# Optimization experiments

Hardware: AMD Instinct MI355X
Metric: run time of the kernel (lower is better)

Reference implementation:

```python
import jax, jax.numpy as jnp
import numpy as np

LN_EPS = 1e-5

def _layernorm(x, w, b):
    mu = jnp.mean(x, axis=-1, keepdims=True)
    var = jnp.mean(jnp.square(x - mu), axis=-1, keepdims=True)
    return (x - mu) * jax.lax.rsqrt(var + LN_EPS) * w + b

def setup_inputs() -> dict:
    key = jax.random.key(0)
    ks = jax.random.split(key, 8)
    B, T, D, E = 8, 4096, 1024, 4
    inner = 4 * D
    x = jax.random.normal(ks[0], (B, T, D), dtype=jnp.float32)
    router_prob = jax.random.uniform(ks[1], (B, T, E), dtype=jnp.float32)
    alpha = jnp.ones((), dtype=jnp.float32)
    norm_w = jnp.ones((D,), dtype=jnp.float32)
    norm_b = jnp.zeros((D,), dtype=jnp.float32)
    l1_w = jax.random.normal(ks[2], (inner, D), dtype=jnp.float32) * 0.02
    l1_b = jax.random.normal(ks[3], (inner,), dtype=jnp.float32) * 0.02
    l2_w = jax.random.normal(ks[4], (D, inner), dtype=jnp.float32) * 0.02
    l2_b = jax.random.normal(ks[5], (D,), dtype=jnp.float32) * 0.02
    return {"x": x, "router_prob": router_prob, "alpha": alpha,
            "norm_w": norm_w, "norm_b": norm_b,
            "l1_w": l1_w, "l1_b": l1_b, "l2_w": l2_w, "l2_b": l2_b}

def reference(x, router_prob, alpha, norm_w, norm_b, l1_w, l1_b, l2_w, l2_b):
    B, T, D = x.shape
    E = router_prob.shape[2]
    n = T // E  # tokens per expert (contiguous slices)
    outs = []
    for e in range(E):  # small fixed loop; each expert has a different width m
        xs = x[:, e * n:(e + 1) * n, :]              # [B,n,D]
        h = _layernorm(xs, norm_w, norm_b)
        m = D // (2 ** e)                             # Matryoshka width
        he = h[:, :, :m]                              # [B,n,m]
        # dropout is a no-op in eval mode
        inner = jax.nn.gelu(jnp.einsum('btm,im->bti', he, l1_w[:, :m]) + l1_b,
                            approximate=False)        # [B,n,4D]
        out = jnp.einsum('bti,mi->btm', inner, l2_w[:m, :]) + l2_b[:m]  # [B,n,m]
        out = jnp.pad(out, ((0, 0), (0, 0), (0, D - m)))
        scale = alpha * router_prob[:, e * n:(e + 1) * n, e] + 1.0      # [B,n]
        outs.append(xs + scale[:, :, None] * out)
    return jnp.concatenate(outs, axis=1)
```

## Files before the change

### kernel.cpp

```cpp
#include <hip/hip_runtime.h>
#include <cstdint>

#define DD     1024
#define NINNER 4096
#define NTOK   32768
#define MROWS  8192

typedef unsigned short u16;
typedef __bf16 bf16x8 __attribute__((ext_vector_type(8)));
typedef float  f32x4  __attribute__((ext_vector_type(4)));

__device__ __forceinline__ u16 f2bf(float f) {
    union { float f; uint32_t u; } a; a.f = f;
    uint32_t r = a.u + 0x7fffu + ((a.u >> 16) & 1u);
    return (u16)(r >> 16);
}

__device__ __forceinline__ void async16(const void* g, void* l) {
    __builtin_amdgcn_global_load_lds(
        (const __attribute__((address_space(1))) void*)g,
        (__attribute__((address_space(3))) void*)l,
        16, 0, 0);
}

#define BARRIER() do { asm volatile("" ::: "memory");              \
                       __builtin_amdgcn_s_barrier();               \
                       asm volatile("" ::: "memory"); } while (0)

__global__ __launch_bounds__(256) void cast_w(
    const float* __restrict__ w1, const float* __restrict__ w2,
    u16* __restrict__ w1b, u16* __restrict__ w2b)
{
    int idx = blockIdx.x * 256 + threadIdx.x;
    const int n1 = (NINNER * DD) / 4;
    float4 v; ushort4 o;
    if (idx < n1) {
        v = ((const float4*)w1)[idx];
        o.x = f2bf(v.x); o.y = f2bf(v.y); o.z = f2bf(v.z); o.w = f2bf(v.w);
        ((ushort4*)w1b)[idx] = o;
    } else {
        int j = idx - n1;
        v = ((const float4*)w2)[j];
        o.x = f2bf(v.x); o.y = f2bf(v.y); o.z = f2bf(v.z); o.w = f2bf(v.w);
        ((ushort4*)w2b)[j] = o;
    }
}

__global__ __launch_bounds__(256) void ln_kernel(
    const float* __restrict__ x, const float* __restrict__ nw,
    const float* __restrict__ nb, const float* __restrict__ l2b,
    const float* __restrict__ rp, const float* __restrict__ alphap,
    u16* __restrict__ h, float* __restrict__ out)
{
    const int row = blockIdx.x;
    const int tid = threadIdx.x;
    const float4 v = ((const float4*)(x + (size_t)row * DD))[tid];
    float s  = v.x + v.y + v.z + v.w;
    float s2 = v.x*v.x + v.y*v.y + v.z*v.z + v.w*v.w;
#pragma unroll
    for (int o = 32; o > 0; o >>= 1) {
        s  += __shfl_down(s,  o, 64);
        s2 += __shfl_down(s2, o, 64);
    }
    __shared__ float as1[4], as2[4];
    if ((tid & 63) == 0) { as1[tid >> 6] = s; as2[tid >> 6] = s2; }
    __syncthreads();
    const float S  = as1[0] + as1[1] + as1[2] + as1[3];
    const float S2 = as2[0] + as2[1] + as2[2] + as2[3];
    const float mu  = S  * (1.0f / 1024.0f);
    const float var = S2 * (1.0f / 1024.0f) - mu * mu;
    const float rs  = rsqrtf(var + 1e-5f);
    const float4 w4 = ((const float4*)nw)[tid];
    const float4 b4 = ((const float4*)nb)[tid];
    ushort4 hv;
    hv.x = f2bf((v.x - mu) * rs * w4.x + b4.x);
    hv.y = f2bf((v.y - mu) * rs * w4.y + b4.y);
    hv.z = f2bf((v.z - mu) * rs * w4.z + b4.z);
    hv.w = f2bf((v.w - mu) * rs * w4.w + b4.w);
    ((ushort4*)(h + (size_t)row * DD))[tid] = hv;

    const int e = (row >> 10) & 3;
    const int m = DD >> e;
    float4 o4;
    if (tid * 4 < m) {
        const float sc = alphap[0] * rp[(size_t)row * 4 + e] + 1.0f;
        const float4 lb = ((const float4*)l2b)[tid];
        o4.x = v.x + sc * lb.x; o4.y = v.y + sc * lb.y;
        o4.z = v.z + sc * lb.z; o4.w = v.w + sc * lb.w;
    } else {
        o4 = v;
    }
    ((float4*)(out + (size_t)row * DD))[tid] = o4;
}

__global__ __launch_bounds__(256) void gemm1(
    const u16* __restrict__ h, const u16* __restrict__ w1b,
    const float* __restrict__ l1b, u16* __restrict__ inner,
    int K, int e)
{
    __shared__ __align__(16) u16 lA[128 * 64];
    __shared__ __align__(16) u16 lB[128 * 64];
    const int tid  = threadIdx.x;
    const int lane = tid & 63;
    const int w    = tid >> 6;
    const int wr   = w >> 1, wc = w & 1;
    const int bm = blockIdx.y, bn = blockIdx.x;

    f32x4 acc[4][4] = {};

    const int srow = (lane >> 3);
    const int soff = ((lane & 7) ^ srow) * 8;

    for (int kt = 0; kt < K; kt += 64) {
#pragma unroll
        for (int i = 0; i < 4; ++i) {
            const int c   = w * 4 + i;
            const int row = c * 8 + srow;
            const int rl  = bm * 128 + row;
            const int g   = ((rl >> 10) << 12) + (e << 10) + (rl & 1023);
            async16(h + (size_t)g * DD + kt + soff, &lA[c * 512]);
        }
#pragma unroll
        for (int i = 0; i < 4; ++i) {
            const int c   = w * 4 + i;
            const int row = c * 8 + srow;
            async16(w1b + (size_t)(bn * 128 + row) * DD + kt + soff, &lB[c * 512]);
        }
        __syncthreads();
#pragma unroll
        for (int kk = 0; kk < 2; ++kk) {
            const int sg = ((kk * 4 + (lane >> 4)) ^ (lane & 7)) * 8;
            bf16x8 af[4], bq[4];
#pragma unroll
            for (int i = 0; i < 4; ++i)
                af[i] = *(const bf16x8*)&lA[(wr * 64 + i * 16 + (lane & 15)) * 64 + sg];
#pragma unroll
            for (int i = 0; i < 4; ++i)
                bq[i] = *(const bf16x8*)&lB[(wc * 64 + i * 16 + (lane & 15)) * 64 + sg];
#pragma unroll
            for (int mi = 0; mi < 4; ++mi)
#pragma unroll
                for (int ni = 0; ni < 4; ++ni)
                    acc[mi][ni] = __builtin_amdgcn_mfma_f32_16x16x32_bf16(
                        af[mi], bq[ni], acc[mi][ni], 0, 0, 0);
        }
        __syncthreads();
    }

    const int cbase = bn * 128 + wc * 64 + (lane & 15);
    const int rbase = bm * 128 + wr * 64 + (lane >> 4) * 4;
#pragma unroll
    for (int ni = 0; ni < 4; ++ni) {
        const int col = cbase + ni * 16;
        const float bias = l1b[col];
#pragma unroll
        for (int mi = 0; mi < 4; ++mi) {
            const int r0 = rbase + mi * 16;
#pragma unroll
            for (int r = 0; r < 4; ++r) {
                const float vv = acc[mi][ni][r] + bias;
                const float gg = 0.5f * vv * (1.0f + erff(vv * 0.7071067811865476f));
                inner[(size_t)(r0 + r) * NINNER + col] = f2bf(gg);
            }
        }
    }
}

__global__ __launch_bounds__(512, 2) void gemm1_big(
    const u16* __restrict__ h, const u16* __restrict__ w1b,
    const float* __restrict__ l1b, u16* __restrict__ inner,
    int K, int e)
{
    __shared__ __align__(16) u16 lA[2][2][8192];
    __shared__ __align__(16) u16 lB[2][2][8192];
    const int tid  = threadIdx.x;
    const int lane = tid & 63;
    const int w    = tid >> 6;
    const int qr   = w >> 2;
    const int qc   = w & 3;
    const int l15  = lane & 15, l4g = lane >> 4, l7 = lane & 7;
    const int lrow = lane >> 3;
    const int soff = (l7 ^ lrow) * 8;

    const int id  = blockIdx.x;
    const int swz = (id & 7) * 64 + (id >> 3);
    const int bm  = swz >> 4, bn = swz & 15;

    const int NT = K >> 6;

    size_t aOff[2][2], bOff[2][2];
#pragma unroll
    for (int hf = 0; hf < 2; ++hf)
#pragma unroll
        for (int i = 0; i < 2; ++i) {
            const int c  = i * 8 + w;
            const int rl = bm * 256 + hf * 128 + c * 8 + lrow;
            const int g  = ((rl >> 10) << 12) + (e << 10) + (rl & 1023);
            aOff[hf][i]  = (size_t)g * DD + soff;
            const int rb = bn * 256 + hf * 128 + c * 8 + lrow;
            bOff[hf][i]  = (size_t)rb * DD + soff;
        }

    f32x4 acc[4][4][2] = {};
    bf16x8 af[4][2], bq[2][2];

    auto STAGE_ALL = [&](int buf, int kt) {
        async16(h   + aOff[0][0] + kt, &lA[buf][0][w * 512]);
        async16(h   + aOff[0][1] + kt, &lA[buf][0][(8 + w) * 512]);
        async16(w1b + bOff[0][0] + kt, &lB[buf][0][w * 512]);
        async16(w1b + bOff[0][1] + kt, &lB[buf][0][(8 + w) * 512]);
        async16(w1b + bOff[1][0] + kt, &lB[buf][1][w * 512]);
        async16(w1b + bOff[1][1] + kt, &lB[buf][1][(8 + w) * 512]);
        async16(h   + aOff[1][0] + kt, &lA[buf][1][w * 512]);
        async16(h   + aOff[1][1] + kt, &lA[buf][1][(8 + w) * 512]);
    };
    auto DSA = [&](int buf, int half) {
#pragma unroll
        for (int mi = 0; mi < 4; ++mi)
#pragma unroll
            for (int kk = 0; kk < 2; ++kk)
                af[mi][kk] = *(const bf16x8*)&lA[buf][half]
                    [(qr * 64 + mi * 16 + l15) * 64 + ((kk * 4 + l4g) ^ l7) * 8];
    };
    auto DSB = [&](int buf, int half) {
#pragma unroll
        for (int ni = 0; ni < 2; ++ni)
#pragma unroll
            for (int kk = 0; kk < 2; ++kk)
                bq[ni][kk] = *(const bf16x8*)&lB[buf][half]
                    [(qc * 32 + ni * 16 + l15) * 64 + ((kk * 4 + l4g) ^ l7) * 8];
    };
    auto MM = [&](f32x4 (&ac)[4][2]) {
#pragma unroll
        for (int mi = 0; mi < 4; ++mi)
#pragma unroll
            for (int ni = 0; ni < 2; ++ni) {
                f32x4 c = ac[mi][ni];
                c = __builtin_amdgcn_mfma_f32_16x16x32_bf16(af[mi][0], bq[ni][0], c, 0, 0, 0);
                c = __builtin_amdgcn_mfma_f32_16x16x32_bf16(af[mi][1], bq[ni][1], c, 0, 0, 0);
                ac[mi][ni] = c;
            }
    };

    STAGE_ALL(0, 0);
    asm volatile("s_waitcnt vmcnt(4)" ::: "memory");
    BARRIER();

    for (int t = 0; t < NT; ++t) {
        const int cur = t & 1, nxt = cur ^ 1;
        const int kn  = (t + 1 < NT ? t + 1 : t) << 6;
        STAGE_ALL(nxt, kn);
        DSA(cur, 0);
        DSB(cur, 0);
        __builtin_amdgcn_s_setprio(1);
        MM(acc[0]);
        __builtin_amdgcn_s_setprio(0);
        asm volatile("s_waitcnt vmcnt(10)" ::: "memory");
        BARRIER();
        DSB(cur, 1);
        __builtin_amdgcn_s_setprio(1);
        MM(acc[1]);
        __builtin_amdgcn_s_setprio(0);
        asm volatile("s_waitcnt vmcnt(8)" ::: "memory");
        BARRIER();
        DSA(cur, 1);
        DSB(cur, 0);
        __builtin_amdgcn_s_setprio(1);
        MM(acc[2]);
        __builtin_amdgcn_s_setprio(0);
        DSB(cur, 1);
        __builtin_amdgcn_s_setprio(1);
        MM(acc[3]);
        __builtin_amdgcn_s_setprio(0);
        asm volatile("s_waitcnt vmcnt(4)" ::: "memory");
        BARRIER();
    }

#pragma unroll
    for (int nh = 0; nh < 2; ++nh) {
#pragma unroll
        for (int ni = 0; ni < 2; ++ni) {
            const int col  = bn * 256 + nh * 128 + qc * 32 + ni * 16 + l15;
            const float bias = l1b[col];
#pragma unroll
            for (int mh = 0; mh < 2; ++mh) {
                const int rb = bm * 256 + mh * 128 + qr * 64 + l4g * 4;
#pragma unroll
                for (int mi = 0; mi < 4; ++mi) {
#pragma unroll
                    for (int r = 0; r < 4; ++r) {
                        const float vv = acc[mh * 2 + nh][mi][ni][r] + bias;
                        const float gg = 0.5f * vv * (1.0f + erff(vv * 0.7071067811865476f));
                        inner[(size_t)(rb + mi * 16 + r) * NINNER + col] = f2bf(gg);
                    }
                }
            }
        }
    }
}

template<int BM, int NBUF>
__global__ __launch_bounds__(BM * 2, 2) void gemm2_nk(
    const u16* __restrict__ inner, const u16* __restrict__ w2b,
    const float* __restrict__ rp, const float* __restrict__ alphap,
    float* __restrict__ out, int e, int lgBn)
{
    constexpr int WAVES = BM / 32;
    constexpr int LB    = 512 / BM;
    constexpr int NT    = NINNER / 64;

    __shared__ __align__(16) u16 lA[NBUF][BM * 64];
    __shared__ __align__(16) u16 lB[NBUF][128 * 64];

    const int tid  = threadIdx.x;
    const int lane = tid & 63;
    const int w    = tid >> 6;
    const int wr   = w >> 1, wc = w & 1;
    const int l15  = lane & 15, l4g = lane >> 4, l7 = lane & 7;
    const int lrow = lane >> 3;
    const int soff = (l7 ^ lrow) * 8;

    const int id  = blockIdx.x;
    const int xcd = id & 7, j = id >> 3;
    const int bm  = ((j >> lgBn) << 3) | xcd;
    const int bn  = j & ((1 << lgBn) - 1);

    size_t aOff[4], bOff[LB];
#pragma unroll
    for (int i = 0; i < 4; ++i) {
        const int row = bm * BM + (i * WAVES + w) * 8 + lrow;
        aOff[i] = (size_t)row * NINNER + soff;
    }
#pragma unroll
    for (int i = 0; i < LB; ++i) {
        const int row = bn * 128 + (i * WAVES + w) * 8 + lrow;
        bOff[i] = (size_t)row * NINNER + soff;
    }

    auto STAGE = [&](int buf, int kt) {
#pragma unroll
        for (int i = 0; i < 4; ++i)
            async16(inner + aOff[i] + kt, &lA[buf][(i * WAVES + w) * 512]);
#pragma unroll
        for (int i = 0; i < LB; ++i)
            async16(w2b + bOff[i] + kt, &lB[buf][(i * WAVES + w) * 512]);
    };

    f32x4 acc[4][4] = {};
    bf16x8 af[4][2], bq[4][2];

    STAGE(0, 0);
    if constexpr (NBUF == 3) STAGE(1, 64);
    if constexpr (BM == 256)      asm volatile("s_waitcnt vmcnt(6)"  ::: "memory");
    else if constexpr (BM == 64)  asm volatile("s_waitcnt vmcnt(12)" ::: "memory");
    else                          asm volatile("s_waitcnt vmcnt(0)"  ::: "memory");
    BARRIER();

    int cur = 0, stg = NBUF - 1;
    for (int t = 0; t < NT; ++t) {
        const int ts = (t + NBUF - 1 < NT ? t + NBUF - 1 : NT - 1);
        STAGE(stg, ts * 64);
#pragma unroll
        for (int mi = 0; mi < 4; ++mi)
#pragma unroll
            for (int kk = 0; kk < 2; ++kk)
                af[mi][kk] = *(const bf16x8*)&lA[cur]
                    [(wr * 64 + mi * 16 + l15) * 64 + ((kk * 4 + l4g) ^ l7) * 8];
#pragma unroll
        for (int ni = 0; ni < 4; ++ni)
#pragma unroll
            for (int kk = 0; kk < 2; ++kk)
                bq[ni][kk] = *(const bf16x8*)&lB[cur]
                    [(wc * 64 + ni * 16 + l15) * 64 + ((kk * 4 + l4g) ^ l7) * 8];
        __builtin_amdgcn_s_setprio(1);
#pragma unroll
        for (int mi = 0; mi < 4; ++mi)
#pragma unroll
            for (int ni = 0; ni < 4; ++ni) {
                f32x4 c = acc[mi][ni];
                c = __builtin_amdgcn_mfma_f32_16x16x32_bf16(af[mi][0], bq[ni][0], c, 0, 0, 0);
                c = __builtin_amdgcn_mfma_f32_16x16x32_bf16(af[mi][1], bq[ni][1], c, 0, 0, 0);
                acc[mi][ni] = c;
            }
        __builtin_amdgcn_s_setprio(0);
        if constexpr (BM == 256)      asm volatile("s_waitcnt vmcnt(6)"  ::: "memory");
        else if constexpr (BM == 64)  asm volatile("s_waitcnt vmcnt(12)" ::: "memory");
        else                          asm volatile("s_waitcnt vmcnt(0)"  ::: "memory");
        BARRIER();
        cur = (cur + 1 == NBUF) ? 0 : cur + 1;
        stg = (stg + 1 == NBUF) ? 0 : stg + 1;
    }

    const float alpha = alphap[0];
#pragma unroll
    for (int mi = 0; mi < 4; ++mi) {
#pragma unroll
        for (int r = 0; r < 4; ++r) {
            const int rl = bm * BM + wr * 64 + mi * 16 + l4g * 4 + r;
            const int g  = ((rl >> 10) << 12) + (e << 10) + (rl & 1023);
            const float sc = alpha * rp[(size_t)g * 4 + e] + 1.0f;
            float* po = out + (size_t)g * DD;
#pragma unroll
            for (int ni = 0; ni < 4; ++ni) {
                const int col = bn * 128 + wc * 64 + ni * 16 + l15;
                po[col] += sc * acc[mi][ni][r];
            }
        }
    }
}

extern "C" void kernel_launch(void* const* d_in, const int* in_sizes, int n_in,
                              void* d_out, int out_size, void* d_ws, size_t ws_size,
                              hipStream_t stream) {
    const float* x     = (const float*)d_in[0];
    const float* rp    = (const float*)d_in[1];
    const float* alpha = (const float*)d_in[2];
    const float* nw    = (const float*)d_in[3];
    const float* nb    = (const float*)d_in[4];
    const float* l1w   = (const float*)d_in[5];
    const float* l1b   = (const float*)d_in[6];
    const float* l2w   = (const float*)d_in[7];
    const float* l2b   = (const float*)d_in[8];
    float* out = (float*)d_out;

    char* ws = (char*)d_ws;
    if (ws_size < ((size_t)144 << 20)) return;
    u16* h     = (u16*)(ws);
    u16* inner = (u16*)(ws + ((size_t)64 << 20));
    u16* w1b   = (u16*)(ws + ((size_t)128 << 20));
    u16* w2b   = (u16*)(ws + ((size_t)136 << 20));

    cast_w<<<8192, 256, 0, stream>>>(l1w, l2w, w1b, w2b);
    ln_kernel<<<NTOK, 256, 0, stream>>>(x, nw, nb, l2b, rp, alpha, h, out);
    for (int e = 0; e < 4; ++e) {
        const int m = DD >> e;
        if (e < 2)
            gemm1_big<<<512, 512, 0, stream>>>(h, w1b, l1b, inner, m, e);
        else
            gemm1<<<dim3(NINNER / 128, MROWS / 128), 256, 0, stream>>>(h, w1b, l1b, inner, m, e);
        switch (e) {
            case 0: gemm2_nk<256, 3><<<256, 512, 0, stream>>>(inner, w2b, rp, alpha, out, e, 3); break;
            case 1: gemm2_nk<128, 2><<<256, 256, 0, stream>>>(inner, w2b, rp, alpha, out, e, 2); break;
            case 2: gemm2_nk< 64, 3><<<256, 128, 0, stream>>>(inner, w2b, rp, alpha, out, e, 1); break;
            case 3: gemm2_nk< 64, 3><<<128, 128, 0, stream>>>(inner, w2b, rp, alpha, out, e, 0); break;
        }
    }
}
```

Baseline: 893.2 us.

## Restructure big GEMM1 into 8-phase half-tile pipeline and use polynomial GELU

Result: faster. 855.3 us (-4.2%).

```diff
diff --git a/kernel.cpp b/kernel.cpp
--- a/kernel.cpp
+++ b/kernel.cpp
@@ -14,6 +14,20 @@
     union { float f; uint32_t u; } a; a.f = f;
     uint32_t r = a.u + 0x7fffu + ((a.u >> 16) & 1u);
     return (u16)(r >> 16);
+}
+
+__device__ __forceinline__ float gelu_f(float v) {
+    const float xs = v * 0.7071067811865476f;
+    const float ax = fabsf(xs);
+    const float t  = 1.0f / (1.0f + 0.3275911f * ax);
+    float p = 1.061405429f;
+    p = fmaf(p, t, -1.453152027f);
+    p = fmaf(p, t,  1.421413741f);
+    p = fmaf(p, t, -0.284496736f);
+    p = fmaf(p, t,  0.254829592f);
+    const float er = 1.0f - p * t * __expf(-ax * ax);
+    const float erf_xs = (xs < 0.0f) ? -er : er;
+    return 0.5f * v * (1.0f + erf_xs);
 }
 
 __device__ __forceinline__ void async16(const void* g, void* l) {
@@ -157,16 +171,24 @@
         for (int mi = 0; mi < 4; ++mi) {
             const int r0 = rbase + mi * 16;
 #pragma unroll
-            for (int r = 0; r < 4; ++r) {
-                const float vv = acc[mi][ni][r] + bias;
-                const float gg = 0.5f * vv * (1.0f + erff(vv * 0.7071067811865476f));
-                inner[(size_t)(r0 + r) * NINNER + col] = f2bf(gg);
-            }
-        }
-    }
-}
-
-__global__ __launch_bounds__(512, 2) void gemm1_big(
+            for (int r = 0; r < 4; ++r)
+                inner[(size_t)(r0 + r) * NINNER + col] = f2bf(gelu_f(acc[mi][ni][r] + bias));
+        }
+    }
+}
+
+#define PH_MID() do { __builtin_amdgcn_s_barrier();                         \
+                      asm volatile("s_waitcnt lgkmcnt(0)" ::: "memory");    \
+                      __builtin_amdgcn_sched_barrier(0);                    \
+                      __builtin_amdgcn_s_setprio(1); } while (0)
+#define PH_END() do { __builtin_amdgcn_s_setprio(0);                        \
+                      asm volatile("" ::: "memory");                        \
+                      __builtin_amdgcn_s_barrier(); } while (0)
+#define PH_END_GATE() do { __builtin_amdgcn_s_setprio(0);                   \
+                      asm volatile("s_waitcnt vmcnt(4)" ::: "memory");      \
+                      __builtin_amdgcn_s_barrier(); } while (0)
+
+__global__ __launch_bounds__(512, 2) void gemm1_8p(
     const u16* __restrict__ h, const u16* __restrict__ w1b,
     const float* __restrict__ l1b, u16* __restrict__ inner,
     int K, int e)
@@ -187,6 +209,7 @@
     const int bm  = swz >> 4, bn = swz & 15;
 
     const int NT = K >> 6;
+    const int NI = NT >> 1;
 
     size_t aOff[2][2], bOff[2][2];
 #pragma unroll
@@ -202,17 +225,17 @@
         }
 
     f32x4 acc[4][4][2] = {};
-    bf16x8 af[4][2], bq[2][2];
-
-    auto STAGE_ALL = [&](int buf, int kt) {
-        async16(h   + aOff[0][0] + kt, &lA[buf][0][w * 512]);
-        async16(h   + aOff[0][1] + kt, &lA[buf][0][(8 + w) * 512]);
-        async16(w1b + bOff[0][0] + kt, &lB[buf][0][w * 512]);
-        async16(w1b + bOff[0][1] + kt, &lB[buf][0][(8 + w) * 512]);
-        async16(w1b + bOff[1][0] + kt, &lB[buf][1][w * 512]);
-        async16(w1b + bOff[1][1] + kt, &lB[buf][1][(8 + w) * 512]);
-        async16(h   + aOff[1][0] + kt, &lA[buf][1][w * 512]);
-        async16(h   + aOff[1][1] + kt, &lA[buf][1][(8 + w) * 512]);
+    bf16x8 af[4][2], bq0[2][2], bq1[2][2];
+
+    auto STA = [&](int buf, int half, int t) {
+        const int kt = t << 6;
+        async16(h + aOff[half][0] + kt, &lA[buf][half][w * 512]);
+        async16(h + aOff[half][1] + kt, &lA[buf][half][(8 + w) * 512]);
+    };
+    auto STB = [&](int buf, int half, int t) {
+        const int kt = t << 6;
+        async16(w1b + bOff[half][0] + kt, &lB[buf][half][w * 512]);
+        async16(w1b + bOff[half][1] + kt, &lB[buf][half][(8 + w) * 512]);
     };
     auto DSA = [&](int buf, int half) {
 #pragma unroll
@@ -222,7 +245,7 @@
                 af[mi][kk] = *(const bf16x8*)&lA[buf][half]
                     [(qr * 64 + mi * 16 + l15) * 64 + ((kk * 4 + l4g) ^ l7) * 8];
     };
-    auto DSB = [&](int buf, int half) {
+    auto DSB = [&](int buf, int half, bf16x8 (&bq)[2][2]) {
 #pragma unroll
         for (int ni = 0; ni < 2; ++ni)
 #pragma unroll
@@ -230,50 +253,43 @@
                 bq[ni][kk] = *(const bf16x8*)&lB[buf][half]
                     [(qc * 32 + ni * 16 + l15) * 64 + ((kk * 4 + l4g) ^ l7) * 8];
     };
-    auto MM = [&](f32x4 (&ac)[4][2]) {
+    auto MM = [&](int q, bf16x8 (&bq)[2][2]) {
 #pragma unroll
         for (int mi = 0; mi < 4; ++mi)
 #pragma unroll
             for (int ni = 0; ni < 2; ++ni) {
-                f32x4 c = ac[mi][ni];
+                f32x4 c = acc[q][mi][ni];
                 c = __builtin_amdgcn_mfma_f32_16x16x32_bf16(af[mi][0], bq[ni][0], c, 0, 0, 0);
                 c = __builtin_amdgcn_mfma_f32_16x16x32_bf16(af[mi][1], bq[ni][1], c, 0, 0, 0);
-                ac[mi][ni] = c;
+                acc[q][mi][ni] = c;
             }
     };
 
-    STAGE_ALL(0, 0);
+    STA(0, 0, 0); STB(0, 0, 0); STA(0, 1, 0); STB(0, 1, 0);
+    STA(1, 0, 1); STB(1, 0, 1);
     asm volatile("s_waitcnt vmcnt(4)" ::: "memory");
     BARRIER();
 
-    for (int t = 0; t < NT; ++t) {
-        const int cur = t & 1, nxt = cur ^ 1;
-        const int kn  = (t + 1 < NT ? t + 1 : t) << 6;
-        STAGE_ALL(nxt, kn);
-        DSA(cur, 0);
-        DSB(cur, 0);
-        __builtin_amdgcn_s_setprio(1);
-        MM(acc[0]);
-        __builtin_amdgcn_s_setprio(0);
-        asm volatile("s_waitcnt vmcnt(10)" ::: "memory");
-        BARRIER();
-        DSB(cur, 1);
-        __builtin_amdgcn_s_setprio(1);
-        MM(acc[1]);
-        __builtin_amdgcn_s_setprio(0);
-        asm volatile("s_waitcnt vmcnt(8)" ::: "memory");
-        BARRIER();
-        DSA(cur, 1);
-        DSB(cur, 0);
-        __builtin_amdgcn_s_setprio(1);
-        MM(acc[2]);
-        __builtin_amdgcn_s_setprio(0);
-        DSB(cur, 1);
-        __builtin_amdgcn_s_setprio(1);
-        MM(acc[3]);
-        __builtin_amdgcn_s_setprio(0);
-        asm volatile("s_waitcnt vmcnt(4)" ::: "memory");
-        BARRIER();
+    for (int i = 0; i < NI; ++i) {
+        const int t1  = 2 * i + 1;
+        const int tn0 = (2 * i + 2 < NT) ? 2 * i + 2 : NT - 1;
+        const int tn1 = (2 * i + 3 < NT) ? 2 * i + 3 : NT - 1;
+        DSA(0, 0); DSB(0, 0, bq0); STA(1, 1, t1);
+        PH_MID(); MM(0, bq0); PH_END();
+        DSB(0, 1, bq1); STB(1, 1, t1);
+        PH_MID(); MM(1, bq1); PH_END();
+        DSA(0, 1); STA(0, 0, tn0);
+        PH_MID(); MM(2, bq0); PH_END();
+        STB(0, 0, tn0);
+        PH_MID(); MM(3, bq1); PH_END_GATE();
+        DSA(1, 0); DSB(1, 0, bq0); STA(0, 1, tn0); STB(0, 1, tn0);
+        PH_MID(); MM(0, bq0); PH_END();
+        DSB(1, 1, bq1);
+        PH_MID(); MM(1, bq1); PH_END();
+        DSA(1, 1); STA(1, 0, tn1);
+        PH_MID(); MM(2, bq0); PH_END();
+        STB(1, 0, tn1);
+        PH_MID(); MM(3, bq1); PH_END_GATE();
     }
 
 #pragma unroll
@@ -290,8 +306,7 @@
 #pragma unroll
                     for (int r = 0; r < 4; ++r) {
                         const float vv = acc[mh * 2 + nh][mi][ni][r] + bias;
-                        const float gg = 0.5f * vv * (1.0f + erff(vv * 0.7071067811865476f));
-                        inner[(size_t)(rb + mi * 16 + r) * NINNER + col] = f2bf(gg);
+                        inner[(size_t)(rb + mi * 16 + r) * NINNER + col] = f2bf(gelu_f(vv));
                     }
                 }
             }
@@ -435,7 +450,7 @@
     for (int e = 0; e < 4; ++e) {
         const int m = DD >> e;
         if (e < 2)
-            gemm1_big<<<512, 512, 0, stream>>>(h, w1b, l1b, inner, m, e);
+            gemm1_8p<<<512, 512, 0, stream>>>(h, w1b, l1b, inner, m, e);
         else
             gemm1<<<dim3(NINNER / 128, MROWS / 128), 256, 0, stream>>>(h, w1b, l1b, inner, m, e);
         switch (e) {
```
